# Kernel optimization log

Hardware: AMD Instinct MI355X
Metric: run time of the kernel (lower is better)

The kernel has to match this reference:

```python
import jax, jax.numpy as jnp
import numpy as np
import math

NUM_BUCKETS = 32
MAX_DISTANCE = 128.0
LOG_BASE = 2.0


def relative_position_bucket(delta):
    # delta: float array. Mirrors torch version exactly.
    sign = jnp.sign(delta)
    n = jnp.clip(jnp.abs(delta), 1e-6, MAX_DISTANCE)
    log_index = jnp.floor(jnp.log(n) / math.log(LOG_BASE)).astype(jnp.int32)
    log_index = jnp.clip(log_index, 0, NUM_BUCKETS - 1)
    return log_index * sign.astype(jnp.int32) + (NUM_BUCKETS - 1)


def setup_inputs() -> dict:
    key = jax.random.key(0)
    ks = jax.random.split(key, 16)
    B, G, D, H = 4, 1024, 512, 8
    d_head = D // H
    inp = {
        "query": jax.random.normal(ks[0], (B, G, D), jnp.float32),
        "key": jax.random.normal(ks[1], (B, G, D), jnp.float32),
        "value": jax.random.normal(ks[2], (B, G, D), jnp.float32),
        # 2D coordinates spread over ~[-192, 192] so many log buckets are hit
        "coords": jax.random.normal(ks[3], (B, G, 2), jnp.float32) * 64.0,
        "mask": jax.random.randint(ks[4], (B, G), 0, 2, jnp.int32),
        # Linear params (torch convention: y = x @ W.T + b)
        "Wq": jax.random.normal(ks[5], (D, D), jnp.float32) / np.sqrt(D),
        "bq": jnp.zeros((D,), jnp.float32),
        "Wk": jax.random.normal(ks[6], (D, D), jnp.float32) / np.sqrt(D),
        "bk": jnp.zeros((D,), jnp.float32),
        "Wv": jax.random.normal(ks[7], (D, D), jnp.float32) / np.sqrt(D),
        "bv": jnp.zeros((D,), jnp.float32),
        "Wo": jax.random.normal(ks[8], (D, D), jnp.float32) / np.sqrt(D),
        "bo": jnp.zeros((D,), jnp.float32),
        # relative-position bias tables: (2*num_buckets - 1, num_heads)
        "rpe_x": jax.random.normal(ks[9], (2 * NUM_BUCKETS - 1, H), jnp.float32) * 0.02,
        "rpe_y": jax.random.normal(ks[10], (2 * NUM_BUCKETS - 1, H), jnp.float32) * 0.02,
    }
    return inp


def reference(query, key, value, coords, mask,
              Wq, bq, Wk, bk, Wv, bv, Wo, bo, rpe_x, rpe_y):
    B, Gq, D = query.shape
    Gk = key.shape[1]
    H = rpe_x.shape[1]
    d_head = D // H

    # projections -> (B, H, G, d_head)
    def proj(x, W, b, G):
        return (x @ W.T + b).reshape(B, G, H, d_head).transpose(0, 2, 1, 3)

    Q = proj(query, Wq, bq, Gq)
    K = proj(key, Wk, bk, Gk)
    V = proj(value, Wv, bv, Gk)

    scores = jnp.einsum('bhqd,bhkd->bhqk', Q, K) / math.sqrt(d_head)

    # relative-position bias from 2D coords
    delta = coords[:, :Gq, None, :] - coords[:, None, :Gk, :]  # (B, Gq, Gk, 2)
    bucket_x = relative_position_bucket(delta[..., 0])
    bucket_y = relative_position_bucket(delta[..., 1])
    rpe_bias = rpe_x[bucket_x] + rpe_y[bucket_y]               # (B, Gq, Gk, H)
    scores = scores + rpe_bias.transpose(0, 3, 1, 2)

    scores = jnp.where(mask[:, None, None, :] == 0, -jnp.inf, scores)
    attn = jax.nn.softmax(scores, axis=-1)
    out = jnp.einsum('bhqk,bhkd->bhqd', attn, V)
    out = out.transpose(0, 2, 1, 3).reshape(B, Gq, D)
    return out @ Wo.T + bo
```

## Files before the change

### kernel.cpp

```cpp
#include <hip/hip_runtime.h>
#include <hip/hip_bf16.h>

typedef __attribute__((ext_vector_type(8))) short bf16x8;
typedef __attribute__((ext_vector_type(4))) float f32x4;

__device__ __forceinline__ unsigned short f2bf(float x) {
  union { __hip_bfloat16 h; unsigned short u; } cv;
  cv.h = __float2bfloat16(x);
  return cv.u;
}

__device__ __forceinline__ void gload16(const void* g, void* l) {
  __builtin_amdgcn_global_load_lds(
      (const __attribute__((address_space(1))) unsigned int*)g,
      (__attribute__((address_space(3))) unsigned int*)l, 16, 0, 0);
}

__device__ __forceinline__ int swz128(int row, int colb) {
  return row * 128 + (colb ^ ((row & 7) << 4));
}

__global__ __launch_bounds__(256)
void k_cvt_all(const float* __restrict__ q, const float* __restrict__ k,
               const float* __restrict__ v, const float* __restrict__ Wq,
               const float* __restrict__ Wk, const float* __restrict__ Wv,
               const float* __restrict__ Wo,
               unsigned short* __restrict__ XQ, unsigned short* __restrict__ XK,
               unsigned short* __restrict__ XV, unsigned short* __restrict__ WQB,
               unsigned short* __restrict__ WKB, unsigned short* __restrict__ WVB,
               unsigned short* __restrict__ WOB)
{
  long i = ((long)blockIdx.x * 256 + threadIdx.x) * 8;
  const float* s; unsigned short* d; long off;
  if (i < 2097152)      { s = q; d = XQ; off = i; }
  else if (i < 4194304) { s = k; d = XK; off = i - 2097152; }
  else if (i < 6291456) { s = v; d = XV; off = i - 4194304; }
  else {
    long j = i - 6291456;
    int wsel = (int)(j >> 18);
    off = j & 262143;
    s = wsel == 0 ? Wq : wsel == 1 ? Wk : wsel == 2 ? Wv : Wo;
    d = wsel == 0 ? WQB : wsel == 1 ? WKB : wsel == 2 ? WVB : WOB;
  }
  float4 a = *(const float4*)(s + off);
  float4 bb = *(const float4*)(s + off + 4);
  bf16x8 o;
  o[0] = (short)f2bf(a.x);  o[1] = (short)f2bf(a.y);
  o[2] = (short)f2bf(a.z);  o[3] = (short)f2bf(a.w);
  o[4] = (short)f2bf(bb.x); o[5] = (short)f2bf(bb.y);
  o[6] = (short)f2bf(bb.z); o[7] = (short)f2bf(bb.w);
  *(bf16x8*)(d + off) = o;
}

__device__ __forceinline__ int rbucket(float dd) {
  float ad = fabsf(dd);
  float n = fminf(fmaxf(ad, 1e-6f), 128.0f);
  int li = (int)floorf(logf(n) * 1.4426950408889634f);
  li = li < 0 ? 0 : (li > 31 ? 31 : li);
  int s = (dd > 0.f) ? 1 : ((dd < 0.f) ? -1 : 0);
  return li * s + 31;
}

__global__ __launch_bounds__(256)
void k_buckets(const float* __restrict__ coords, unsigned short* __restrict__ buk) {
  int b = blockIdx.y;
  int f = blockIdx.x * 256 + threadIdx.x;
  int qi = f >> 10, ki = f & 1023;
  const float* cb = coords + (b << 11);
  float qx = cb[qi * 2], qy = cb[qi * 2 + 1];
  float kx = cb[ki * 2], ky = cb[ki * 2 + 1];
  int bx = rbucket(qx - kx);
  int by = rbucket(qy - ky);
  buk[((long)b << 20) + f] = (unsigned short)(bx | (by << 8));
}

__device__ __forceinline__ void gemm_core(
    const unsigned short* __restrict__ A, const unsigned short* __restrict__ Bw,
    int m0, int n0, unsigned short* ldsA, unsigned short* ldsB, f32x4 acc[4][4])
{
  const int t = threadIdx.x;
  const int lane = t & 63;
  const int w = t >> 6;
  const int wm = (w >> 1) << 6;
  const int wn = (w & 1) << 6;
  const int l15 = lane & 15;
  const int l4 = lane >> 4;
  const f32x4 fz = {0.f, 0.f, 0.f, 0.f};

  #pragma unroll
  for (int r = 0; r < 4; ++r)
    #pragma unroll
    for (int c = 0; c < 4; ++c) acc[r][c] = fz;

  for (int k0 = 0; k0 < 512; k0 += 32) {
    #pragma unroll
    for (int rr = 0; rr < 2; ++rr) {
      int c = rr * 256 + t;
      int row = c >> 2, cc = c & 3;
      gload16(A + (m0 + row) * 512 + k0 + cc * 8, (char*)ldsA + c * 16);
      gload16(Bw + (n0 + row) * 512 + k0 + cc * 8, (char*)ldsB + c * 16);
    }
    __syncthreads();
    bf16x8 af[4], bfr[4];
    #pragma unroll
    for (int r = 0; r < 4; ++r) {
      af[r]  = *(const bf16x8*)((const char*)ldsA + (wm + r * 16 + l15) * 64 + l4 * 16);
      bfr[r] = *(const bf16x8*)((const char*)ldsB + (wn + r * 16 + l15) * 64 + l4 * 16);
    }
    #pragma unroll
    for (int r = 0; r < 4; ++r)
      #pragma unroll
      for (int c = 0; c < 4; ++c)
        acc[r][c] = __builtin_amdgcn_mfma_f32_16x16x32_bf16(af[r], bfr[c], acc[r][c], 0, 0, 0);
    __syncthreads();
  }
}

__global__ __launch_bounds__(256)
void k_gemm_proj(const unsigned short* __restrict__ XQ, const unsigned short* __restrict__ XK,
                 const unsigned short* __restrict__ XV, const unsigned short* __restrict__ WQ,
                 const unsigned short* __restrict__ WK, const unsigned short* __restrict__ WV,
                 const float* __restrict__ bq, const float* __restrict__ bk,
                 const float* __restrict__ bv,
                 unsigned short* __restrict__ QP, unsigned short* __restrict__ KP,
                 unsigned short* __restrict__ VT)
{
  __shared__ unsigned short ldsA[128 * 32];
  __shared__ unsigned short ldsB[128 * 32];
  int z = blockIdx.z;
  const unsigned short* A = z == 0 ? XQ : z == 1 ? XK : XV;
  const unsigned short* W = z == 0 ? WQ : z == 1 ? WK : WV;
  const float* bias = z == 0 ? bq : z == 1 ? bk : bv;
  unsigned short* dst = z == 0 ? QP : z == 1 ? KP : VT;
  int m0 = blockIdx.x * 128, n0 = blockIdx.y * 128;
  f32x4 acc[4][4];
  gemm_core(A, W, m0, n0, ldsA, ldsB, acc);

  const int t = threadIdx.x, lane = t & 63, w = t >> 6;
  const int wm = (w >> 1) << 6, wn = (w & 1) << 6;
  const int l15 = lane & 15, l4 = lane >> 4;
  #pragma unroll
  for (int r = 0; r < 4; ++r)
    #pragma unroll
    for (int c = 0; c < 4; ++c)
      #pragma unroll
      for (int i = 0; i < 4; ++i) {
        int m = m0 + wm + r * 16 + (l4 << 2) + i;
        int n = n0 + wn + c * 16 + l15;
        float y = acc[r][c][i] + bias[n];
        int b = m >> 10, g = m & 1023, hh = n >> 6, dd = n & 63;
        dst[((((b << 3) + hh) << 10) + g) * 64 + dd] = f2bf(y);
      }
}

__global__ __launch_bounds__(256)
void k_transp(const unsigned short* __restrict__ src, unsigned short* __restrict__ dst) {
  __shared__ unsigned short tile[64][70];
  int bh = blockIdx.y;
  int g0 = blockIdx.x << 6;
  int t = threadIdx.x;
  int gr = t >> 6;
  int c = t & 63;
  #pragma unroll
  for (int rr = 0; rr < 16; ++rr) {
    int g = (rr << 2) + gr;
    tile[g][c] = src[(((long)bh << 10) + g0 + g) * 64 + c];
  }
  __syncthreads();
  #pragma unroll
  for (int rr = 0; rr < 16; ++rr) {
    int d = (rr << 2) + gr;
    dst[(((long)bh << 6) + d) * 1024 + g0 + c] = tile[c][d];
  }
}

__global__ __launch_bounds__(256)
void k_attn(const unsigned short* __restrict__ QP, const unsigned short* __restrict__ KP,
            const unsigned short* __restrict__ VPT, const unsigned short* __restrict__ BUK,
            const int* __restrict__ mask, const float* __restrict__ rpe_x,
            const float* __restrict__ rpe_y, unsigned short* __restrict__ AO)
{
  __shared__ unsigned short Qs[64 * 64];
  __shared__ unsigned short Ks[64 * 64];
  __shared__ unsigned short Vs[64 * 64];
  __shared__ unsigned short Ps[4 * 16 * 64];
  __shared__ float rx[63], ry[63];

  const int t = threadIdx.x;
  const int lane = t & 63;
  const int w = t >> 6;
  const int l15 = lane & 15;
  const int l4 = lane >> 4;
  const int bh = blockIdx.y;
  const int b = bh >> 3, h = bh & 7;
  const int q0 = blockIdx.x << 6;
  const f32x4 fz = {0.f, 0.f, 0.f, 0.f};

  const unsigned short* Qg = QP + ((long)((bh << 10) + q0)) * 64;
  const unsigned short* Kg = KP + ((long)(bh << 10)) * 64;
  const unsigned short* Vg = VPT + ((long)(bh << 6)) * 1024;
  const int* maskb = mask + (b << 10);
  const unsigned short* bkb = BUK + ((long)b << 20);

  #pragma unroll
  for (int rr = 0; rr < 2; ++rr) {
    int c = rr * 256 + t;
    int row = c >> 3, cc = c & 7;
    int gcc = cc ^ (row & 7);
    gload16(Qg + row * 64 + gcc * 8, (char*)Qs + c * 16);
  }
  if (t < 63) { rx[t] = rpe_x[t * 8 + h]; ry[t] = rpe_y[t * 8 + h]; }
  __syncthreads();

  bf16x8 qf[2];
  #pragma unroll
  for (int ks = 0; ks < 2; ++ks)
    qf[ks] = *(const bf16x8*)((const char*)Qs + swz128((w << 4) + l15, ks * 64 + l4 * 16));

  float mrun[4], lrun[4];
  f32x4 oacc[4];
  #pragma unroll
  for (int i = 0; i < 4; ++i) { mrun[i] = -1e30f; lrun[i] = 0.f; }
  #pragma unroll
  for (int dj = 0; dj < 4; ++dj) oacc[dj] = fz;

  for (int kt = 0; kt < 1024; kt += 64) {
    #pragma unroll
    for (int rr = 0; rr < 2; ++rr) {
      int c = rr * 256 + t;
      int row = c >> 3, cc = c & 7;
      int gcc = cc ^ (row & 7);
      gload16(Kg + (kt + row) * 64 + gcc * 8, (char*)Ks + c * 16);
      gload16(Vg + row * 1024 + kt + gcc * 8, (char*)Vs + c * 16);
    }
    int mk[4];
    #pragma unroll
    for (int nj = 0; nj < 4; ++nj) mk[nj] = maskb[kt + nj * 16 + l15];
    unsigned short bko[4][4];
    #pragma unroll
    for (int i = 0; i < 4; ++i) {
      int qrow = q0 + (w << 4) + (l4 << 2) + i;
      #pragma unroll
      for (int nj = 0; nj < 4; ++nj)
        bko[i][nj] = bkb[((long)qrow << 10) + kt + nj * 16 + l15];
    }
    __syncthreads();

    f32x4 sacc[4];
    #pragma unroll
    for (int nj = 0; nj < 4; ++nj) sacc[nj] = fz;
    #pragma unroll
    for (int nj = 0; nj < 4; ++nj)
      #pragma unroll
      for (int ks = 0; ks < 2; ++ks) {
        bf16x8 kf = *(const bf16x8*)((const char*)Ks + swz128(nj * 16 + l15, ks * 64 + l4 * 16));
        sacc[nj] = __builtin_amdgcn_mfma_f32_16x16x32_bf16(qf[ks], kf, sacc[nj], 0, 0, 0);
      }

    float fsc[4];
    float pv_[4][4];
    #pragma unroll
    for (int i = 0; i < 4; ++i) {
      float sv[4];
      float vm = -1e30f;
      #pragma unroll
      for (int nj = 0; nj < 4; ++nj) {
        unsigned bkv = bko[i][nj];
        float bias = rx[bkv & 255] + ry[bkv >> 8];
        float s = fmaf(sacc[nj][i], 0.125f, bias);
        s = (mk[nj] == 0) ? -1e30f : s;
        sv[nj] = s;
        vm = fmaxf(vm, s);
      }
      vm = fmaxf(vm, __shfl_xor(vm, 1));
      vm = fmaxf(vm, __shfl_xor(vm, 2));
      vm = fmaxf(vm, __shfl_xor(vm, 4));
      vm = fmaxf(vm, __shfl_xor(vm, 8));
      float mo = mrun[i];
      float mn = fmaxf(mo, vm);
      float f = __expf(mo - mn);
      float ps = 0.f;
      #pragma unroll
      for (int nj = 0; nj < 4; ++nj) {
        float p = __expf(sv[nj] - mn);
        pv_[i][nj] = p;
        ps += p;
      }
      ps += __shfl_xor(ps, 1);
      ps += __shfl_xor(ps, 2);
      ps += __shfl_xor(ps, 4);
      ps += __shfl_xor(ps, 8);
      lrun[i] = lrun[i] * f + ps;
      mrun[i] = mn;
      fsc[i] = f;
    }
    #pragma unroll
    for (int dj = 0; dj < 4; ++dj)
      #pragma unroll
      for (int i = 0; i < 4; ++i) oacc[dj][i] *= fsc[i];

    unsigned short* Pw = Ps + (w << 10);
    #pragma unroll
    for (int i = 0; i < 4; ++i) {
      int prow = (l4 << 2) + i;
      #pragma unroll
      for (int nj = 0; nj < 4; ++nj) {
        int pcolb = (nj * 16 + l15) * 2;
        *(unsigned short*)((char*)Pw + swz128(prow, pcolb)) = f2bf(pv_[i][nj]);
      }
    }

    bf16x8 pf[2];
    #pragma unroll
    for (int ks = 0; ks < 2; ++ks)
      pf[ks] = *(const bf16x8*)((const char*)Pw + swz128(l15, ks * 64 + l4 * 16));
    #pragma unroll
    for (int dj = 0; dj < 4; ++dj)
      #pragma unroll
      for (int ks = 0; ks < 2; ++ks) {
        bf16x8 vf = *(const bf16x8*)((const char*)Vs + swz128(dj * 16 + l15, ks * 64 + l4 * 16));
        oacc[dj] = __builtin_amdgcn_mfma_f32_16x16x32_bf16(pf[ks], vf, oacc[dj], 0, 0, 0);
      }
    __syncthreads();
  }

  #pragma unroll
  for (int dj = 0; dj < 4; ++dj)
    #pragma unroll
    for (int i = 0; i < 4; ++i) {
      int g = q0 + (w << 4) + (l4 << 2) + i;
      int dd = dj * 16 + l15;
      float o = oacc[dj][i] / lrun[i];
      AO[((long)((b << 10) + g)) * 512 + h * 64 + dd] = f2bf(o);
    }
}

__global__ __launch_bounds__(256)
void k_gemm_out(const unsigned short* __restrict__ AO, const unsigned short* __restrict__ WO,
                const float* __restrict__ bo, float* __restrict__ out)
{
  __shared__ unsigned short ldsA[128 * 32];
  __shared__ unsigned short ldsB[128 * 32];
  int m0 = blockIdx.x * 128, n0 = blockIdx.y * 128;
  f32x4 acc[4][4];
  gemm_core(AO, WO, m0, n0, ldsA, ldsB, acc);

  const int t = threadIdx.x, lane = t & 63, w = t >> 6;
  const int wm = (w >> 1) << 6, wn = (w & 1) << 6;
  const int l15 = lane & 15, l4 = lane >> 4;
  #pragma unroll
  for (int r = 0; r < 4; ++r)
    #pragma unroll
    for (int c = 0; c < 4; ++c)
      #pragma unroll
      for (int i = 0; i < 4; ++i) {
        int m = m0 + wm + r * 16 + (l4 << 2) + i;
        int n = n0 + wn + c * 16 + l15;
        out[(long)m * 512 + n] = acc[r][c][i] + bo[n];
      }
}

extern "C" void kernel_launch(void* const* d_in, const int* in_sizes, int n_in,
                              void* d_out, int out_size, void* d_ws, size_t ws_size,
                              hipStream_t stream) {
  const float* q      = (const float*)d_in[0];
  const float* k      = (const float*)d_in[1];
  const float* v      = (const float*)d_in[2];
  const float* coords = (const float*)d_in[3];
  const int*   mask   = (const int*)d_in[4];
  const float* Wq     = (const float*)d_in[5];
  const float* bq     = (const float*)d_in[6];
  const float* Wk     = (const float*)d_in[7];
  const float* bk     = (const float*)d_in[8];
  const float* Wv     = (const float*)d_in[9];
  const float* bv     = (const float*)d_in[10];
  const float* Wo     = (const float*)d_in[11];
  const float* bo     = (const float*)d_in[12];
  const float* rpe_x  = (const float*)d_in[13];
  const float* rpe_y  = (const float*)d_in[14];
  float* out = (float*)d_out;

  unsigned short* WQB  = (unsigned short*)d_ws;
  unsigned short* WKB  = WQB + 262144;
  unsigned short* WVB  = WKB + 262144;
  unsigned short* WOB  = WVB + 262144;
  unsigned short* XQ   = WOB + 262144;
  unsigned short* XK   = XQ + 2097152;
  unsigned short* XV   = XK + 2097152;
  unsigned short* QP   = XV + 2097152;
  unsigned short* KP   = QP + 2097152;
  unsigned short* VTMP = KP + 2097152;
  unsigned short* VPT  = VTMP + 2097152;
  unsigned short* AO   = VPT + 2097152;
  unsigned short* BUK  = AO + 2097152;

  k_cvt_all<<<dim3(3584), dim3(256), 0, stream>>>(q, k, v, Wq, Wk, Wv, Wo,
                                                  XQ, XK, XV, WQB, WKB, WVB, WOB);
  k_buckets<<<dim3(4096, 4), dim3(256), 0, stream>>>(coords, BUK);
  k_gemm_proj<<<dim3(32, 4, 3), dim3(256), 0, stream>>>(XQ, XK, XV, WQB, WKB, WVB,
                                                        bq, bk, bv, QP, KP, VTMP);
  k_transp<<<dim3(16, 32), dim3(256), 0, stream>>>(VTMP, VPT);
  k_attn<<<dim3(16, 32), dim3(256), 0, stream>>>(QP, KP, VPT, BUK, mask,
                                                 rpe_x, rpe_y, AO);
  k_gemm_out<<<dim3(32, 4), dim3(256), 0, stream>>>(AO, WOB, bo, out);
}
```

Baseline: 180.6 us.

## Compact unmasked keys and skip masked key tiles in attention

Adds a prefix-scan over the mask to build a compacted index of valid keys per batch, then gathers K and transposed V into compacted buffers and computes bucket indices only for valid keys. The attention kernel loops only over tiles of valid keys, loads K/V fragments directly from global memory without LDS staging or block barriers, and uses an XCD-aware block mapping. Projection and output GEMMs switch to 128x64 tiles for more blocks. Adds extra scan and gather launches and relies on uncoalesced direct global fragment loads in attention.

New measurement: 181.0 us. Within noise of the previous version (+0.3%).

```diff
diff --git a/kernel.cpp b/kernel.cpp
--- a/kernel.cpp
+++ b/kernel.cpp
@@ -52,6 +52,24 @@
   *(bf16x8*)(d + off) = o;
 }
 
+__global__ __launch_bounds__(1024)
+void k_scan(const int* __restrict__ mask, int* __restrict__ idx, int* __restrict__ cnt) {
+  __shared__ int ps[1024];
+  int b = blockIdx.x, t = threadIdx.x;
+  int m = mask[(b << 10) + t];
+  ps[t] = m;
+  __syncthreads();
+  #pragma unroll
+  for (int off = 1; off < 1024; off <<= 1) {
+    int v = (t >= off) ? ps[t - off] : 0;
+    __syncthreads();
+    ps[t] += v;
+    __syncthreads();
+  }
+  if (m) idx[(b << 10) + ps[t] - 1] = t;
+  if (t == 1023) cnt[b] = ps[t];
+}
+
 __device__ __forceinline__ int rbucket(float dd) {
   float ad = fabsf(dd);
   float n = fminf(fmaxf(ad, 1e-6f), 128.0f);
@@ -62,27 +80,65 @@
 }
 
 __global__ __launch_bounds__(256)
-void k_buckets(const float* __restrict__ coords, unsigned short* __restrict__ buk) {
+void k_buckets_c(const float* __restrict__ coords, const int* __restrict__ idx,
+                 const int* __restrict__ cnt, unsigned short* __restrict__ buk) {
   int b = blockIdx.y;
   int f = blockIdx.x * 256 + threadIdx.x;
-  int qi = f >> 10, ki = f & 1023;
+  int qi = f >> 10, ck = f & 1023;
+  if (ck >= cnt[b]) return;
+  int ki = idx[(b << 10) + ck];
   const float* cb = coords + (b << 11);
-  float qx = cb[qi * 2], qy = cb[qi * 2 + 1];
-  float kx = cb[ki * 2], ky = cb[ki * 2 + 1];
-  int bx = rbucket(qx - kx);
-  int by = rbucket(qy - ky);
-  buk[((long)b << 20) + f] = (unsigned short)(bx | (by << 8));
-}
-
-__device__ __forceinline__ void gemm_core(
+  float dx = cb[qi * 2] - cb[ki * 2];
+  float dy = cb[qi * 2 + 1] - cb[ki * 2 + 1];
+  int bx = rbucket(dx);
+  int by = rbucket(dy);
+  buk[((long)(b << 10) + qi) * 1024 + ck] = (unsigned short)(bx | (by << 8));
+}
+
+__global__ __launch_bounds__(256)
+void k_gatherKV(const unsigned short* __restrict__ KP,
+                const unsigned short* __restrict__ VTMP,
+                const int* __restrict__ idx, const int* __restrict__ cnt,
+                unsigned short* __restrict__ KC, unsigned short* __restrict__ VCT)
+{
+  __shared__ unsigned short tile[64][68];
+  __shared__ int lidx[64];
+  int bh = blockIdx.y, b = bh >> 3;
+  int cn = cnt[b];
+  int ck0 = blockIdx.x << 6;
+  if (ck0 >= cn) return;
+  int t = threadIdx.x;
+  if (t < 64) lidx[t] = idx[(b << 10) + min(ck0 + t, cn - 1)];
+  __syncthreads();
+  int r = t >> 2, qd = t & 3;
+  long srcrow = ((long)(bh << 10) + lidx[r]) * 64;
+  long dstrow = ((long)(bh << 10) + ck0 + r) * 64;
+  uint4 kv0 = *(const uint4*)(KP + srcrow + qd * 16);
+  uint4 kv1 = *(const uint4*)(KP + srcrow + qd * 16 + 8);
+  *(uint4*)(KC + dstrow + qd * 16) = kv0;
+  *(uint4*)(KC + dstrow + qd * 16 + 8) = kv1;
+  const uint2* vsrc = (const uint2*)(VTMP + srcrow + qd * 16);
+  #pragma unroll
+  for (int s = 0; s < 4; ++s)
+    *(uint2*)(&tile[r][qd * 16 + s * 4]) = vsrc[s];
+  __syncthreads();
+  #pragma unroll
+  for (int it = 0; it < 16; ++it) {
+    int d = it * 4 + (t >> 6);
+    int ck = t & 63;
+    VCT[((long)(bh << 6) + d) * 1024 + ck0 + ck] = tile[ck][d];
+  }
+}
+
+__device__ __forceinline__ void gemm_core64(
     const unsigned short* __restrict__ A, const unsigned short* __restrict__ Bw,
-    int m0, int n0, unsigned short* ldsA, unsigned short* ldsB, f32x4 acc[4][4])
+    int m0, int n0, unsigned short* ldsA, unsigned short* ldsB, f32x4 acc[4][2])
 {
   const int t = threadIdx.x;
   const int lane = t & 63;
   const int w = t >> 6;
   const int wm = (w >> 1) << 6;
-  const int wn = (w & 1) << 6;
+  const int wn = (w & 1) << 5;
   const int l15 = lane & 15;
   const int l4 = lane >> 4;
   const f32x4 fz = {0.f, 0.f, 0.f, 0.f};
@@ -90,7 +146,7 @@
   #pragma unroll
   for (int r = 0; r < 4; ++r)
     #pragma unroll
-    for (int c = 0; c < 4; ++c) acc[r][c] = fz;
+    for (int c = 0; c < 2; ++c) acc[r][c] = fz;
 
   for (int k0 = 0; k0 < 512; k0 += 32) {
     #pragma unroll
@@ -98,19 +154,24 @@
       int c = rr * 256 + t;
       int row = c >> 2, cc = c & 3;
       gload16(A + (m0 + row) * 512 + k0 + cc * 8, (char*)ldsA + c * 16);
+    }
+    {
+      int c = t;
+      int row = c >> 2, cc = c & 3;
       gload16(Bw + (n0 + row) * 512 + k0 + cc * 8, (char*)ldsB + c * 16);
     }
     __syncthreads();
-    bf16x8 af[4], bfr[4];
-    #pragma unroll
-    for (int r = 0; r < 4; ++r) {
-      af[r]  = *(const bf16x8*)((const char*)ldsA + (wm + r * 16 + l15) * 64 + l4 * 16);
-      bfr[r] = *(const bf16x8*)((const char*)ldsB + (wn + r * 16 + l15) * 64 + l4 * 16);
-    }
+    bf16x8 af[4], bfr[2];
     #pragma unroll
     for (int r = 0; r < 4; ++r)
-      #pragma unroll
-      for (int c = 0; c < 4; ++c)
+      af[r] = *(const bf16x8*)((const char*)ldsA + (wm + r * 16 + l15) * 64 + l4 * 16);
+    #pragma unroll
+    for (int c = 0; c < 2; ++c)
+      bfr[c] = *(const bf16x8*)((const char*)ldsB + (wn + c * 16 + l15) * 64 + l4 * 16);
+    #pragma unroll
+    for (int r = 0; r < 4; ++r)
+      #pragma unroll
+      for (int c = 0; c < 2; ++c)
         acc[r][c] = __builtin_amdgcn_mfma_f32_16x16x32_bf16(af[r], bfr[c], acc[r][c], 0, 0, 0);
     __syncthreads();
   }
@@ -126,23 +187,23 @@
                  unsigned short* __restrict__ VT)
 {
   __shared__ unsigned short ldsA[128 * 32];
-  __shared__ unsigned short ldsB[128 * 32];
+  __shared__ unsigned short ldsB[64 * 32];
   int z = blockIdx.z;
   const unsigned short* A = z == 0 ? XQ : z == 1 ? XK : XV;
   const unsigned short* W = z == 0 ? WQ : z == 1 ? WK : WV;
   const float* bias = z == 0 ? bq : z == 1 ? bk : bv;
   unsigned short* dst = z == 0 ? QP : z == 1 ? KP : VT;
-  int m0 = blockIdx.x * 128, n0 = blockIdx.y * 128;
-  f32x4 acc[4][4];
-  gemm_core(A, W, m0, n0, ldsA, ldsB, acc);
+  int m0 = blockIdx.x * 128, n0 = blockIdx.y * 64;
+  f32x4 acc[4][2];
+  gemm_core64(A, W, m0, n0, ldsA, ldsB, acc);
 
   const int t = threadIdx.x, lane = t & 63, w = t >> 6;
-  const int wm = (w >> 1) << 6, wn = (w & 1) << 6;
+  const int wm = (w >> 1) << 6, wn = (w & 1) << 5;
   const int l15 = lane & 15, l4 = lane >> 4;
   #pragma unroll
   for (int r = 0; r < 4; ++r)
     #pragma unroll
-    for (int c = 0; c < 4; ++c)
+    for (int c = 0; c < 2; ++c)
       #pragma unroll
       for (int i = 0; i < 4; ++i) {
         int m = m0 + wm + r * 16 + (l4 << 2) + i;
@@ -154,68 +215,44 @@
 }
 
 __global__ __launch_bounds__(256)
-void k_transp(const unsigned short* __restrict__ src, unsigned short* __restrict__ dst) {
-  __shared__ unsigned short tile[64][70];
-  int bh = blockIdx.y;
-  int g0 = blockIdx.x << 6;
-  int t = threadIdx.x;
-  int gr = t >> 6;
-  int c = t & 63;
-  #pragma unroll
-  for (int rr = 0; rr < 16; ++rr) {
-    int g = (rr << 2) + gr;
-    tile[g][c] = src[(((long)bh << 10) + g0 + g) * 64 + c];
-  }
-  __syncthreads();
-  #pragma unroll
-  for (int rr = 0; rr < 16; ++rr) {
-    int d = (rr << 2) + gr;
-    dst[(((long)bh << 6) + d) * 1024 + g0 + c] = tile[c][d];
-  }
-}
-
-__global__ __launch_bounds__(256)
-void k_attn(const unsigned short* __restrict__ QP, const unsigned short* __restrict__ KP,
-            const unsigned short* __restrict__ VPT, const unsigned short* __restrict__ BUK,
-            const int* __restrict__ mask, const float* __restrict__ rpe_x,
+void k_attn(const unsigned short* __restrict__ QP, const unsigned short* __restrict__ KC,
+            const unsigned short* __restrict__ VCT, const unsigned short* __restrict__ BUKC,
+            const int* __restrict__ cnt, const float* __restrict__ rpe_x,
             const float* __restrict__ rpe_y, unsigned short* __restrict__ AO)
 {
-  __shared__ unsigned short Qs[64 * 64];
-  __shared__ unsigned short Ks[64 * 64];
-  __shared__ unsigned short Vs[64 * 64];
-  __shared__ unsigned short Ps[4 * 16 * 64];
-  __shared__ float rx[63], ry[63];
+  __shared__ float rx[64], ry[64];
+  __shared__ unsigned short Ps[4][16 * 64];
 
   const int t = threadIdx.x;
   const int lane = t & 63;
   const int w = t >> 6;
   const int l15 = lane & 15;
   const int l4 = lane >> 4;
-  const int bh = blockIdx.y;
-  const int b = bh >> 3, h = bh & 7;
-  const int q0 = blockIdx.x << 6;
   const f32x4 fz = {0.f, 0.f, 0.f, 0.f};
 
-  const unsigned short* Qg = QP + ((long)((bh << 10) + q0)) * 64;
-  const unsigned short* Kg = KP + ((long)(bh << 10)) * 64;
-  const unsigned short* Vg = VPT + ((long)(bh << 6)) * 1024;
-  const int* maskb = mask + (b << 10);
-  const unsigned short* bkb = BUK + ((long)b << 20);
-
-  #pragma unroll
-  for (int rr = 0; rr < 2; ++rr) {
-    int c = rr * 256 + t;
-    int row = c >> 3, cc = c & 7;
-    int gcc = cc ^ (row & 7);
-    gload16(Qg + row * 64 + gcc * 8, (char*)Qs + c * 16);
-  }
+  int g = blockIdx.x;
+  int xcd = g & 7, slot = g >> 3;
+  int b = xcd >> 1;
+  int qb = ((xcd & 1) << 3) | (slot & 7);
+  int h = slot >> 3;
+  int bh = (b << 3) | h;
+  int qw = (qb << 6) | (w << 4);
+
   if (t < 63) { rx[t] = rpe_x[t * 8 + h]; ry[t] = rpe_y[t * 8 + h]; }
+  else if (t == 63) { rx[63] = 0.f; ry[63] = 0.f; }
   __syncthreads();
 
+  const unsigned short* Qg = QP + ((long)(bh << 10) + qw) * 64;
   bf16x8 qf[2];
   #pragma unroll
   for (int ks = 0; ks < 2; ++ks)
-    qf[ks] = *(const bf16x8*)((const char*)Qs + swz128((w << 4) + l15, ks * 64 + l4 * 16));
+    qf[ks] = *(const bf16x8*)(Qg + (long)l15 * 64 + ks * 32 + l4 * 8);
+
+  const int cn = cnt[b];
+  const int nkt = (cn + 63) >> 6;
+  const unsigned short* Kg = KC + ((long)(bh << 10)) * 64;
+  const unsigned short* Vg = VCT + ((long)(bh << 6)) * 1024;
+  const unsigned short* bukb = BUKC + (((long)(b << 10) + qw) << 10);
 
   float mrun[4], lrun[4];
   f32x4 oacc[4];
@@ -224,27 +261,16 @@
   #pragma unroll
   for (int dj = 0; dj < 4; ++dj) oacc[dj] = fz;
 
-  for (int kt = 0; kt < 1024; kt += 64) {
-    #pragma unroll
-    for (int rr = 0; rr < 2; ++rr) {
-      int c = rr * 256 + t;
-      int row = c >> 3, cc = c & 7;
-      int gcc = cc ^ (row & 7);
-      gload16(Kg + (kt + row) * 64 + gcc * 8, (char*)Ks + c * 16);
-      gload16(Vg + row * 1024 + kt + gcc * 8, (char*)Vs + c * 16);
-    }
-    int mk[4];
-    #pragma unroll
-    for (int nj = 0; nj < 4; ++nj) mk[nj] = maskb[kt + nj * 16 + l15];
+  unsigned short* Pw = &Ps[w][0];
+
+  for (int kt = 0; kt < nkt; ++kt) {
+    const int k0 = kt << 6;
     unsigned short bko[4][4];
     #pragma unroll
-    for (int i = 0; i < 4; ++i) {
-      int qrow = q0 + (w << 4) + (l4 << 2) + i;
+    for (int i = 0; i < 4; ++i)
       #pragma unroll
       for (int nj = 0; nj < 4; ++nj)
-        bko[i][nj] = bkb[((long)qrow << 10) + kt + nj * 16 + l15];
-    }
-    __syncthreads();
+        bko[i][nj] = bukb[(((long)((l4 << 2) + i)) << 10) + k0 + nj * 16 + l15];
 
     f32x4 sacc[4];
     #pragma unroll
@@ -253,7 +279,7 @@
     for (int nj = 0; nj < 4; ++nj)
       #pragma unroll
       for (int ks = 0; ks < 2; ++ks) {
-        bf16x8 kf = *(const bf16x8*)((const char*)Ks + swz128(nj * 16 + l15, ks * 64 + l4 * 16));
+        bf16x8 kf = *(const bf16x8*)(Kg + (long)(k0 + nj * 16 + l15) * 64 + ks * 32 + l4 * 8);
         sacc[nj] = __builtin_amdgcn_mfma_f32_16x16x32_bf16(qf[ks], kf, sacc[nj], 0, 0, 0);
       }
 
@@ -266,9 +292,9 @@
       #pragma unroll
       for (int nj = 0; nj < 4; ++nj) {
         unsigned bkv = bko[i][nj];
-        float bias = rx[bkv & 255] + ry[bkv >> 8];
+        float bias = rx[bkv & 63] + ry[(bkv >> 8) & 63];
         float s = fmaf(sacc[nj][i], 0.125f, bias);
-        s = (mk[nj] == 0) ? -1e30f : s;
+        s = ((k0 + nj * 16 + l15) < cn) ? s : -1e30f;
         sv[nj] = s;
         vm = fmaxf(vm, s);
       }
@@ -299,7 +325,6 @@
       #pragma unroll
       for (int i = 0; i < 4; ++i) oacc[dj][i] *= fsc[i];
 
-    unsigned short* Pw = Ps + (w << 10);
     #pragma unroll
     for (int i = 0; i < 4; ++i) {
       int prow = (l4 << 2) + i;
@@ -309,29 +334,28 @@
         *(unsigned short*)((char*)Pw + swz128(prow, pcolb)) = f2bf(pv_[i][nj]);
       }
     }
-
     bf16x8 pf[2];
     #pragma unroll
     for (int ks = 0; ks < 2; ++ks)
       pf[ks] = *(const bf16x8*)((const char*)Pw + swz128(l15, ks * 64 + l4 * 16));
+
     #pragma unroll
     for (int dj = 0; dj < 4; ++dj)
       #pragma unroll
       for (int ks = 0; ks < 2; ++ks) {
-        bf16x8 vf = *(const bf16x8*)((const char*)Vs + swz128(dj * 16 + l15, ks * 64 + l4 * 16));
+        bf16x8 vf = *(const bf16x8*)(Vg + (long)(dj * 16 + l15) * 1024 + k0 + ks * 32 + l4 * 8);
         oacc[dj] = __builtin_amdgcn_mfma_f32_16x16x32_bf16(pf[ks], vf, oacc[dj], 0, 0, 0);
       }
-    __syncthreads();
   }
 
   #pragma unroll
   for (int dj = 0; dj < 4; ++dj)
     #pragma unroll
     for (int i = 0; i < 4; ++i) {
-      int g = q0 + (w << 4) + (l4 << 2) + i;
+      int gq = qw + (l4 << 2) + i;
       int dd = dj * 16 + l15;
       float o = oacc[dj][i] / lrun[i];
-      AO[((long)((b << 10) + g)) * 512 + h * 64 + dd] = f2bf(o);
+      AO[((long)((b << 10) + gq)) * 512 + h * 64 + dd] = f2bf(o);
     }
 }
 
@@ -340,18 +364,18 @@
                 const float* __restrict__ bo, float* __restrict__ out)
 {
   __shared__ unsigned short ldsA[128 * 32];
-  __shared__ unsigned short ldsB[128 * 32];
-  int m0 = blockIdx.x * 128, n0 = blockIdx.y * 128;
-  f32x4 acc[4][4];
-  gemm_core(AO, WO, m0, n0, ldsA, ldsB, acc);
+  __shared__ unsigned short ldsB[64 * 32];
+  int m0 = blockIdx.x * 128, n0 = blockIdx.y * 64;
+  f32x4 acc[4][2];
+  gemm_core64(AO, WO, m0, n0, ldsA, ldsB, acc);
 
   const int t = threadIdx.x, lane = t & 63, w = t >> 6;
-  const int wm = (w >> 1) << 6, wn = (w & 1) << 6;
+  const int wm = (w >> 1) << 6, wn = (w & 1) << 5;
   const int l15 = lane & 15, l4 = lane >> 4;
   #pragma unroll
   for (int r = 0; r < 4; ++r)
     #pragma unroll
-    for (int c = 0; c < 4; ++c)
+    for (int c = 0; c < 2; ++c)
       #pragma unroll
       for (int i = 0; i < 4; ++i) {
         int m = m0 + wm + r * 16 + (l4 << 2) + i;
@@ -390,17 +414,21 @@
   unsigned short* QP   = XV + 2097152;
   unsigned short* KP   = QP + 2097152;
   unsigned short* VTMP = KP + 2097152;
-  unsigned short* VPT  = VTMP + 2097152;
-  unsigned short* AO   = VPT + 2097152;
-  unsigned short* BUK  = AO + 2097152;
+  unsigned short* KC   = VTMP + 2097152;
+  unsigned short* VCT  = KC + 2097152;
+  unsigned short* AO   = VCT + 2097152;
+  int* idxp            = (int*)(AO + 2097152);
+  int* cntp            = idxp + 4096;
+  unsigned short* BUKC = XQ;
 
   k_cvt_all<<<dim3(3584), dim3(256), 0, stream>>>(q, k, v, Wq, Wk, Wv, Wo,
                                                   XQ, XK, XV, WQB, WKB, WVB, WOB);
-  k_buckets<<<dim3(4096, 4), dim3(256), 0, stream>>>(coords, BUK);
-  k_gemm_proj<<<dim3(32, 4, 3), dim3(256), 0, stream>>>(XQ, XK, XV, WQB, WKB, WVB,
+  k_scan<<<dim3(4), dim3(1024), 0, stream>>>(mask, idxp, cntp);
+  k_gemm_proj<<<dim3(32, 8, 3), dim3(256), 0, stream>>>(XQ, XK, XV, WQB, WKB, WVB,
                                                         bq, bk, bv, QP, KP, VTMP);
-  k_transp<<<dim3(16, 32), dim3(256), 0, stream>>>(VTMP, VPT);
-  k_attn<<<dim3(16, 32), dim3(256), 0, stream>>>(QP, KP, VPT, BUK, mask,
-                                                 rpe_x, rpe_y, AO);
-  k_gemm_out<<<dim3(32, 4), dim3(256), 0, stream>>>(AO, WOB, bo, out);
-}
+  k_gatherKV<<<dim3(16, 32), dim3(256), 0, stream>>>(KP, VTMP, idxp, cntp, KC, VCT);
+  k_buckets_c<<<dim3(4096, 4), dim3(256), 0, stream>>>(coords, idxp, cntp, BUKC);
+  k_attn<<<dim3(512), dim3(256), 0, stream>>>(QP, KC, VCT, BUKC, cntp,
+                                              rpe_x, rpe_y, AO);
+  k_gemm_out<<<dim3(32, 8), dim3(256), 0, stream>>>(AO, WOB, bo, out);
+}
```
